# Kernel tuning notes

Measured on AMD Instinct MI355X. Metric: run time of the kernel, lower is better.

## Reference

```python
import jax, jax.numpy as jnp
import numpy as np

N_NODES = 50000
N_EDGES = 600000
IN_F = 128
HID_F = 128
OUT_F = 128


def setup_inputs() -> dict:
    key = jax.random.key(0)
    ks = jax.random.split(key, 12)
    features = jax.random.normal(ks[0], (N_NODES, IN_F), dtype=jnp.float32)
    src = jax.random.randint(ks[1], (N_EDGES,), 0, N_NODES, dtype=jnp.int32)
    dst = jax.random.randint(ks[2], (N_EDGES,), 0, N_NODES, dtype=jnp.int32)

    def lin(k, fan_in, fan_out):
        s = 1.0 / jnp.sqrt(fan_in)
        return jax.random.uniform(k, (fan_in, fan_out), jnp.float32, -s, s)

    return {
        "features": features, "src": src, "dst": dst,
        "W1_self": lin(ks[3], IN_F, HID_F), "W1_neigh": lin(ks[4], IN_F, HID_F),
        "b1": jnp.zeros((HID_F,), jnp.float32),
        "W2_self": lin(ks[5], HID_F, HID_F), "W2_neigh": lin(ks[6], HID_F, HID_F),
        "b2": jnp.zeros((HID_F,), jnp.float32),
        "W3_self": lin(ks[7], HID_F, OUT_F), "W3_neigh": lin(ks[8], HID_F, OUT_F),
        "b3": jnp.zeros((OUT_F,), jnp.float32),
    }


def _sage_mean(x, src, dst, W_self, W_neigh, b):
    # gather source-node features along edges, mean-reduce into dst nodes
    msgs = x[src]                                                # [E, d]
    summed = jax.ops.segment_sum(msgs, dst, num_segments=N_NODES)  # [N, d]
    deg = jax.ops.segment_sum(jnp.ones((dst.shape[0],), x.dtype), dst,
                              num_segments=N_NODES)               # [N]
    mean = summed / jnp.maximum(deg, 1.0)[:, None]
    return x @ W_self + mean @ W_neigh + b


def reference(features, src, dst,
              W1_self, W1_neigh, b1,
              W2_self, W2_neigh, b2,
              W3_self, W3_neigh, b3):
    x = features.reshape(features.shape[0], -1)  # Flatten (no-op for 2D)
    x = jax.nn.relu(_sage_mean(x, src, dst, W1_self, W1_neigh, b1))
    x = jax.nn.relu(_sage_mean(x, src, dst, W2_self, W2_neigh, b2))
    x = _sage_mean(x, src, dst, W3_self, W3_neigh, b3)
    return x
```

## Files before the change

kernel.cpp:

```cpp
#include <hip/hip_runtime.h>

#define NN 50000
#define NE 600000
#define F 128

typedef __attribute__((ext_vector_type(4))) float f4;
typedef __attribute__((ext_vector_type(4))) float f32x4;
typedef __bf16 bf16x8 __attribute__((ext_vector_type(8)));
typedef short short8v __attribute__((ext_vector_type(8)));
typedef unsigned short u16x4 __attribute__((ext_vector_type(4)));

__device__ inline ushort f2bf(float f) {
    uint u = __builtin_bit_cast(uint, f);
    uint r = (u + 0x7FFFu + ((u >> 16) & 1u)) >> 16;
    return (ushort)r;
}
__device__ inline float bf2f(ushort u) {
    uint t = ((uint)u) << 16;
    return __builtin_bit_cast(float, t);
}


__global__ void count_deg(const int* __restrict__ dst, int* __restrict__ deg, int E) {
    int e = blockIdx.x * blockDim.x + threadIdx.x;
    if (e < E) atomicAdd(&deg[dst[e]], 1);
}

__global__ __launch_bounds__(1024) void scan_part1(const int* __restrict__ deg,
                                                   int* __restrict__ bsum, int N) {
    __shared__ int ws[16];
    int tid = threadIdx.x;
    int idx = blockIdx.x * 1024 + tid;
    int v = (idx < N) ? deg[idx] : 0;
    #pragma unroll
    for (int o = 32; o; o >>= 1) v += __shfl_down(v, o);
    if ((tid & 63) == 0) ws[tid >> 6] = v;
    __syncthreads();
    if (tid < 64) {
        int t = (tid < 16) ? ws[tid] : 0;
        #pragma unroll
        for (int o = 8; o; o >>= 1) t += __shfl_down(t, o);
        if (tid == 0) bsum[blockIdx.x] = t;
    }
}

__global__ void scan_part2(int* __restrict__ bsum, int nb) {
    int lane = threadIdx.x;
    int v = (lane < nb) ? bsum[lane] : 0;
    int x = v;
    #pragma unroll
    for (int o = 1; o < 64; o <<= 1) {
        int t = __shfl_up(x, o);
        if (lane >= o) x += t;
    }
    if (lane < nb) bsum[lane] = x - v;
}

__global__ __launch_bounds__(1024) void scan_part3(const int* __restrict__ deg,
                                                   const int* __restrict__ bsum,
                                                   int* __restrict__ off,
                                                   int* __restrict__ cur,
                                                   float* __restrict__ recip, int N) {
    __shared__ int wsum[16];
    int tid = threadIdx.x;
    int wid = tid >> 6;
    int lane = tid & 63;
    int idx = blockIdx.x * 1024 + tid;
    int v = (idx < N) ? deg[idx] : 0;
    int x = v;
    #pragma unroll
    for (int o = 1; o < 64; o <<= 1) {
        int t = __shfl_up(x, o);
        if (lane >= o) x += t;
    }
    if (lane == 63) wsum[wid] = x;
    __syncthreads();
    if (tid == 0) {
        int a = 0;
        #pragma unroll
        for (int w = 0; w < 16; ++w) { int t = wsum[w]; wsum[w] = a; a += t; }
    }
    __syncthreads();
    int incl = x + wsum[wid];
    if (idx < N) {
        int start = bsum[blockIdx.x] + incl - v;
        off[idx] = start;
        cur[idx] = start;
        recip[idx] = 1.0f / (float)max(v, 1);
    }
}

__global__ void fill_csr(const int* __restrict__ src, const int* __restrict__ dst,
                         int* __restrict__ cur, int* __restrict__ csr, int E) {
    int e = blockIdx.x * blockDim.x + threadIdx.x;
    if (e < E) {
        int pos = atomicAdd(&cur[dst[e]], 1);
        csr[pos] = src[e];
    }
}


__global__ __launch_bounds__(256) void wt_prep(const float* __restrict__ W1s, const float* __restrict__ W1n,
                                               const float* __restrict__ W2s, const float* __restrict__ W2n,
                                               const float* __restrict__ W3s, const float* __restrict__ W3n,
                                               ushort* __restrict__ Bt1, ushort* __restrict__ Bt2,
                                               ushort* __restrict__ Bt3) {
    int layer = blockIdx.y;
    const float* Ws = (layer == 0) ? W1s : (layer == 1) ? W2s : W3s;
    const float* Wn = (layer == 0) ? W1n : (layer == 1) ? W2n : W3n;
    ushort* Bt = (layer == 0) ? Bt1 : (layer == 1) ? Bt2 : Bt3;
    int col = blockIdx.x;
    int k = threadIdx.x;
    float v = (k < 128) ? Ws[k * 128 + col] : Wn[(k - 128) * 128 + col];
    Bt[col * 256 + k] = f2bf(v);
}


__global__ __launch_bounds__(256) void to_bf16(const float* __restrict__ in,
                                               ushort* __restrict__ out, int n8) {
    int i = blockIdx.x * 256 + threadIdx.x;
    if (i < n8) {
        const f4* p = (const f4*)in + (size_t)i * 2;
        f4 a = p[0], b = p[1];
        short8v w;
        w[0] = (short)f2bf(a[0]); w[1] = (short)f2bf(a[1]);
        w[2] = (short)f2bf(a[2]); w[3] = (short)f2bf(a[3]);
        w[4] = (short)f2bf(b[0]); w[5] = (short)f2bf(b[1]);
        w[6] = (short)f2bf(b[2]); w[7] = (short)f2bf(b[3]);
        ((short8v*)out)[i] = w;
    }
}


__global__ __launch_bounds__(256) void agg_mean(const ushort* __restrict__ xb,
                                                const int* __restrict__ off,
                                                const int* __restrict__ deg,
                                                const float* __restrict__ recip,
                                                const int* __restrict__ csr,
                                                ushort* __restrict__ meanb, int N) {
    int node = blockIdx.x * 8 + (threadIdx.x >> 5);
    if (node >= N) return;
    int lane = threadIdx.x & 31;
    int start = off[node];
    int d = deg[node];
    const u16x4* xp = (const u16x4*)xb;
    f4 a = (f4)0.f;
    int nfull = d & ~7;
    int i = 0;
    for (; i < nfull; i += 8) {
        int s[8];
        #pragma unroll
        for (int u = 0; u < 8; ++u) s[u] = csr[start + i + u];
        u16x4 v[8];
        #pragma unroll
        for (int u = 0; u < 8; ++u) v[u] = xp[(size_t)s[u] * 32 + lane];
        #pragma unroll
        for (int u = 0; u < 8; ++u) {
            a[0] += bf2f(v[u][0]); a[1] += bf2f(v[u][1]);
            a[2] += bf2f(v[u][2]); a[3] += bf2f(v[u][3]);
        }
    }
    if (i < d) {
        int dm1 = d - 1;
        int s[8];
        #pragma unroll
        for (int u = 0; u < 8; ++u) {
            int idx = i + u;
            s[u] = csr[start + ((idx < dm1) ? idx : dm1)];
        }
        u16x4 v[8];
        #pragma unroll
        for (int u = 0; u < 8; ++u) v[u] = xp[(size_t)s[u] * 32 + lane];
        #pragma unroll
        for (int u = 0; u < 8; ++u) {
            float m = (i + u < d) ? 1.f : 0.f;
            a[0] += m * bf2f(v[u][0]); a[1] += m * bf2f(v[u][1]);
            a[2] += m * bf2f(v[u][2]); a[3] += m * bf2f(v[u][3]);
        }
    }
    float r = recip[node];
    u16x4 o;
    o[0] = f2bf(a[0] * r); o[1] = f2bf(a[1] * r);
    o[2] = f2bf(a[2] * r); o[3] = f2bf(a[3] * r);
    ((u16x4*)meanb)[(size_t)node * 32 + lane] = o;
}


template <int RELU, int OUTBF>
__global__ __launch_bounds__(256) void sage_gemm(const ushort* __restrict__ xb,
                                                 const ushort* __restrict__ meanb,
                                                 const ushort* __restrict__ Bt,
                                                 const float* __restrict__ bias,
                                                 void* __restrict__ outp, int N) {
    __shared__ ushort sa[32 * 256];
    int tid = threadIdx.x;
    int r0 = blockIdx.x * 32;

    {
        int row = tid >> 3;
        int kc = tid & 7;
        int grow = r0 + row;
        const ushort* srcp = (kc < 4) ? &xb[(size_t)grow * 128 + kc * 32]
                                      : &meanb[(size_t)grow * 128 + (kc - 4) * 32];
        uint base = (uint)(row * 512 + kc * 64);
        uint sw = ((uint)row & 7u) << 4;
        #pragma unroll
        for (int c = 0; c < 4; ++c) {
            short8v w;
            if (grow < N) w = ((const short8v*)srcp)[c];
            else          w = (short8v)0;
            *(short8v*)((char*)sa + ((base + c * 16) ^ sw)) = w;
        }
    }
    __syncthreads();

    int lane = tid & 63;
    int wid = tid >> 6;
    int wr = wid & 1;
    int wc = wid >> 1;
    int l15 = lane & 15;
    int lg = lane >> 4;

    int arow = wr * 16 + l15;
    uint abase = (uint)(arow * 512 + lg * 16);
    uint asw = ((uint)arow & 7u) << 4;
    bf16x8 a[8];
    #pragma unroll
    for (int ks = 0; ks < 8; ++ks) {
        a[ks] = *(const bf16x8*)((const char*)sa + ((abase + (uint)ks * 64) ^ asw));
    }

    f32x4 acc[4];
    #pragma unroll
    for (int ct = 0; ct < 4; ++ct) acc[ct] = (f32x4)0.f;

    #pragma unroll
    for (int ct = 0; ct < 4; ++ct) {
        int bcol = wc * 64 + ct * 16 + l15;
        const ushort* bp = Bt + bcol * 256 + lg * 8;
        #pragma unroll
        for (int ks = 0; ks < 8; ++ks) {
            bf16x8 b = *(const bf16x8*)(bp + ks * 32);
            acc[ct] = __builtin_amdgcn_mfma_f32_16x16x32_bf16(a[ks], b, acc[ct], 0, 0, 0);
        }
    }

    int crow = r0 + wr * 16 + lg * 4;
    #pragma unroll
    for (int ct = 0; ct < 4; ++ct) {
        int col = wc * 64 + ct * 16 + l15;
        float bv = bias[col];
        #pragma unroll
        for (int r = 0; r < 4; ++r) {
            int row = crow + r;
            if (row < N) {
                float v = acc[ct][r] + bv;
                if (RELU) v = fmaxf(v, 0.f);
                if (OUTBF) ((ushort*)outp)[(size_t)row * 128 + col] = f2bf(v);
                else       ((float*)outp)[(size_t)row * 128 + col] = v;
            }
        }
    }
}


extern "C" void kernel_launch(void* const* d_in, const int* in_sizes, int n_in,
                              void* d_out, int out_size, void* d_ws, size_t ws_size,
                              hipStream_t stream) {
    const float* feat = (const float*)d_in[0];
    const int* src = (const int*)d_in[1];
    const int* dst = (const int*)d_in[2];
    const float* W1s = (const float*)d_in[3];
    const float* W1n = (const float*)d_in[4];
    const float* b1 = (const float*)d_in[5];
    const float* W2s = (const float*)d_in[6];
    const float* W2n = (const float*)d_in[7];
    const float* b2 = (const float*)d_in[8];
    const float* W3s = (const float*)d_in[9];
    const float* W3n = (const float*)d_in[10];
    const float* b3 = (const float*)d_in[11];
    float* out = (float*)d_out;

    const int N = NN, E = NE;
    const int NB = (N + 1023) / 1024;

    char* p = (char*)d_ws;
    auto alloc = [&](size_t bytes) {
        char* q = p;
        p += (bytes + 255) & ~(size_t)255;
        return q;
    };
    int* deg = (int*)alloc((size_t)N * 4);
    int* off = (int*)alloc((size_t)N * 4);
    int* cur = (int*)alloc((size_t)N * 4);
    float* recip = (float*)alloc((size_t)N * 4);
    int* bsum = (int*)alloc(64 * 4);
    int* csr = (int*)alloc((size_t)E * 4);
    ushort* xb0 = (ushort*)alloc((size_t)N * F * 2);
    ushort* h1b = (ushort*)alloc((size_t)N * F * 2);
    ushort* h2b = (ushort*)alloc((size_t)N * F * 2);
    ushort* meanb = (ushort*)alloc((size_t)N * F * 2);
    ushort* Bt1 = (ushort*)alloc(128 * 256 * 2);
    ushort* Bt2 = (ushort*)alloc(128 * 256 * 2);
    ushort* Bt3 = (ushort*)alloc(128 * 256 * 2);

    wt_prep<<<dim3(128, 3), 256, 0, stream>>>(W1s, W1n, W2s, W2n, W3s, W3n, Bt1, Bt2, Bt3);
    to_bf16<<<(N * F / 8 + 255) / 256, 256, 0, stream>>>(feat, xb0, N * F / 8);

    hipMemsetAsync(deg, 0, (size_t)N * 4, stream);
    count_deg<<<(E + 255) / 256, 256, 0, stream>>>(dst, deg, E);
    scan_part1<<<NB, 1024, 0, stream>>>(deg, bsum, N);
    scan_part2<<<1, 64, 0, stream>>>(bsum, NB);
    scan_part3<<<NB, 1024, 0, stream>>>(deg, bsum, off, cur, recip, N);
    fill_csr<<<(E + 255) / 256, 256, 0, stream>>>(src, dst, cur, csr, E);

    int aggGrid = (N + 7) / 8;
    int gemmGrid = (N + 31) / 32;

    agg_mean<<<aggGrid, 256, 0, stream>>>(xb0, off, deg, recip, csr, meanb, N);
    sage_gemm<1, 1><<<gemmGrid, 256, 0, stream>>>(xb0, meanb, Bt1, b1, h1b, N);
    agg_mean<<<aggGrid, 256, 0, stream>>>(h1b, off, deg, recip, csr, meanb, N);
    sage_gemm<1, 1><<<gemmGrid, 256, 0, stream>>>(h1b, meanb, Bt2, b2, h2b, N);
    agg_mean<<<aggGrid, 256, 0, stream>>>(h2b, off, deg, recip, csr, meanb, N);
    sage_gemm<0, 0><<<gemmGrid, 256, 0, stream>>>(h2b, meanb, Bt3, b3, out, N);
}
```

Baseline: 253.4 us.

## Fuse mean aggregation into SAGE GEMM kernel and fold scan_part2 into scan_part3

Merges the separate mean-aggregation kernel into the GEMM kernel. Each block now gathers neighbour features for its 32 rows straight into shared memory, with 16 lanes per node using 16-byte loads, so the intermediate mean buffer is never written to or read back from global memory. The small scan_part2 launch is removed: each scan_part3 block recomputes the block-prefix over bsum itself. The cost is less parallelism during the gather (16 threads per node inside a GEMM-sized block), and the MFMA work now waits on the irregular gather latency.

```diff
diff --git a/kernel.cpp b/kernel.cpp
--- a/kernel.cpp
+++ b/kernel.cpp
@@ -8,7 +8,7 @@
 typedef __attribute__((ext_vector_type(4))) float f32x4;
 typedef __bf16 bf16x8 __attribute__((ext_vector_type(8)));
 typedef short short8v __attribute__((ext_vector_type(8)));
-typedef unsigned short u16x4 __attribute__((ext_vector_type(4)));
+typedef unsigned short u16x8 __attribute__((ext_vector_type(8)));
 
 __device__ inline ushort f2bf(float f) {
     uint u = __builtin_bit_cast(uint, f);
@@ -44,27 +44,27 @@
     }
 }
 
-__global__ void scan_part2(int* __restrict__ bsum, int nb) {
-    int lane = threadIdx.x;
-    int v = (lane < nb) ? bsum[lane] : 0;
-    int x = v;
-    #pragma unroll
-    for (int o = 1; o < 64; o <<= 1) {
-        int t = __shfl_up(x, o);
-        if (lane >= o) x += t;
-    }
-    if (lane < nb) bsum[lane] = x - v;
-}
-
 __global__ __launch_bounds__(1024) void scan_part3(const int* __restrict__ deg,
                                                    const int* __restrict__ bsum,
                                                    int* __restrict__ off,
                                                    int* __restrict__ cur,
-                                                   float* __restrict__ recip, int N) {
+                                                   float* __restrict__ recip,
+                                                   int N, int NB) {
     __shared__ int wsum[16];
+    __shared__ int sbase;
     int tid = threadIdx.x;
     int wid = tid >> 6;
     int lane = tid & 63;
+    if (tid < 64) {
+        int v = (tid < NB) ? bsum[tid] : 0;
+        int x = v;
+        #pragma unroll
+        for (int o = 1; o < 64; o <<= 1) {
+            int t = __shfl_up(x, o);
+            if (lane >= o) x += t;
+        }
+        if (tid == blockIdx.x) sbase = x - v;
+    }
     int idx = blockIdx.x * 1024 + tid;
     int v = (idx < N) ? deg[idx] : 0;
     int x = v;
@@ -83,7 +83,7 @@
     __syncthreads();
     int incl = x + wsum[wid];
     if (idx < N) {
-        int start = bsum[blockIdx.x] + incl - v;
+        int start = sbase + incl - v;
         off[idx] = start;
         cur[idx] = start;
         recip[idx] = 1.0f / (float)max(v, 1);
@@ -132,84 +132,89 @@
 }
 
 
-__global__ __launch_bounds__(256) void agg_mean(const ushort* __restrict__ xb,
-                                                const int* __restrict__ off,
-                                                const int* __restrict__ deg,
-                                                const float* __restrict__ recip,
-                                                const int* __restrict__ csr,
-                                                ushort* __restrict__ meanb, int N) {
-    int node = blockIdx.x * 8 + (threadIdx.x >> 5);
-    if (node >= N) return;
-    int lane = threadIdx.x & 31;
-    int start = off[node];
-    int d = deg[node];
-    const u16x4* xp = (const u16x4*)xb;
-    f4 a = (f4)0.f;
-    int nfull = d & ~7;
-    int i = 0;
-    for (; i < nfull; i += 8) {
-        int s[8];
-        #pragma unroll
-        for (int u = 0; u < 8; ++u) s[u] = csr[start + i + u];
-        u16x4 v[8];
-        #pragma unroll
-        for (int u = 0; u < 8; ++u) v[u] = xp[(size_t)s[u] * 32 + lane];
-        #pragma unroll
-        for (int u = 0; u < 8; ++u) {
-            a[0] += bf2f(v[u][0]); a[1] += bf2f(v[u][1]);
-            a[2] += bf2f(v[u][2]); a[3] += bf2f(v[u][3]);
-        }
-    }
-    if (i < d) {
-        int dm1 = d - 1;
-        int s[8];
-        #pragma unroll
-        for (int u = 0; u < 8; ++u) {
-            int idx = i + u;
-            s[u] = csr[start + ((idx < dm1) ? idx : dm1)];
-        }
-        u16x4 v[8];
-        #pragma unroll
-        for (int u = 0; u < 8; ++u) v[u] = xp[(size_t)s[u] * 32 + lane];
-        #pragma unroll
-        for (int u = 0; u < 8; ++u) {
-            float m = (i + u < d) ? 1.f : 0.f;
-            a[0] += m * bf2f(v[u][0]); a[1] += m * bf2f(v[u][1]);
-            a[2] += m * bf2f(v[u][2]); a[3] += m * bf2f(v[u][3]);
-        }
-    }
-    float r = recip[node];
-    u16x4 o;
-    o[0] = f2bf(a[0] * r); o[1] = f2bf(a[1] * r);
-    o[2] = f2bf(a[2] * r); o[3] = f2bf(a[3] * r);
-    ((u16x4*)meanb)[(size_t)node * 32 + lane] = o;
-}
-
-
 template <int RELU, int OUTBF>
-__global__ __launch_bounds__(256) void sage_gemm(const ushort* __restrict__ xb,
-                                                 const ushort* __restrict__ meanb,
-                                                 const ushort* __restrict__ Bt,
-                                                 const float* __restrict__ bias,
-                                                 void* __restrict__ outp, int N) {
+__global__ __launch_bounds__(256) void sage_layer(const ushort* __restrict__ xb,
+                                                  const int* __restrict__ off,
+                                                  const int* __restrict__ deg,
+                                                  const float* __restrict__ recip,
+                                                  const int* __restrict__ csr,
+                                                  const ushort* __restrict__ Bt,
+                                                  const float* __restrict__ bias,
+                                                  void* __restrict__ outp, int N) {
     __shared__ ushort sa[32 * 256];
     int tid = threadIdx.x;
     int r0 = blockIdx.x * 32;
 
     {
         int row = tid >> 3;
-        int kc = tid & 7;
+        int c = tid & 7;
         int grow = r0 + row;
-        const ushort* srcp = (kc < 4) ? &xb[(size_t)grow * 128 + kc * 32]
-                                      : &meanb[(size_t)grow * 128 + (kc - 4) * 32];
-        uint base = (uint)(row * 512 + kc * 64);
         uint sw = ((uint)row & 7u) << 4;
-        #pragma unroll
-        for (int c = 0; c < 4; ++c) {
+        uint base = (uint)(row * 512 + c * 32);
+        short8v w0 = (short8v)0, w1 = (short8v)0;
+        if (grow < N) {
+            const short8v* sp = (const short8v*)&xb[(size_t)grow * 128 + c * 16];
+            w0 = sp[0]; w1 = sp[1];
+        }
+        *(short8v*)((char*)sa + (base ^ sw)) = w0;
+        *(short8v*)((char*)sa + ((base + 16) ^ sw)) = w1;
+    }
+
+    {
+        int g = tid >> 4;
+        int l16 = tid & 15;
+        const ushort* xpb = xb + (size_t)l16 * 8;
+        #pragma unroll
+        for (int rep = 0; rep < 2; ++rep) {
+            int row = g + rep * 16;
+            int node = r0 + row;
+            float a[8] = {0.f, 0.f, 0.f, 0.f, 0.f, 0.f, 0.f, 0.f};
+            if (node < N) {
+                int start = off[node];
+                int d = deg[node];
+                int nfull = d & ~7;
+                int i = 0;
+                for (; i < nfull; i += 8) {
+                    int s[8];
+                    #pragma unroll
+                    for (int u = 0; u < 8; ++u) s[u] = csr[start + i + u];
+                    u16x8 v[8];
+                    #pragma unroll
+                    for (int u = 0; u < 8; ++u) v[u] = *(const u16x8*)(xpb + (size_t)s[u] * 128);
+                    #pragma unroll
+                    for (int u = 0; u < 8; ++u) {
+                        #pragma unroll
+                        for (int j = 0; j < 8; ++j) a[j] += bf2f(v[u][j]);
+                    }
+                }
+                if (i < d) {
+                    int dm1 = d - 1;
+                    int s[8];
+                    #pragma unroll
+                    for (int u = 0; u < 8; ++u) {
+                        int idx = i + u;
+                        s[u] = csr[start + ((idx < dm1) ? idx : dm1)];
+                    }
+                    u16x8 v[8];
+                    #pragma unroll
+                    for (int u = 0; u < 8; ++u) v[u] = *(const u16x8*)(xpb + (size_t)s[u] * 128);
+                    #pragma unroll
+                    for (int u = 0; u < 8; ++u) {
+                        float m = (i + u < d) ? 1.f : 0.f;
+                        #pragma unroll
+                        for (int j = 0; j < 8; ++j) a[j] += m * bf2f(v[u][j]);
+                    }
+                }
+                float r = recip[node];
+                #pragma unroll
+                for (int j = 0; j < 8; ++j) a[j] *= r;
+            }
             short8v w;
-            if (grow < N) w = ((const short8v*)srcp)[c];
-            else          w = (short8v)0;
-            *(short8v*)((char*)sa + ((base + c * 16) ^ sw)) = w;
+            #pragma unroll
+            for (int j = 0; j < 8; ++j) w[j] = (short)f2bf(a[j]);
+            uint sw = ((uint)row & 7u) << 4;
+            uint addr = (uint)(row * 512 + 256 + l16 * 16);
+            *(short8v*)((char*)sa + (addr ^ sw)) = w;
         }
     }
     __syncthreads();
@@ -299,7 +304,6 @@
     ushort* xb0 = (ushort*)alloc((size_t)N * F * 2);
     ushort* h1b = (ushort*)alloc((size_t)N * F * 2);
     ushort* h2b = (ushort*)alloc((size_t)N * F * 2);
-    ushort* meanb = (ushort*)alloc((size_t)N * F * 2);
     ushort* Bt1 = (ushort*)alloc(128 * 256 * 2);
     ushort* Bt2 = (ushort*)alloc(128 * 256 * 2);
     ushort* Bt3 = (ushort*)alloc(128 * 256 * 2);
@@ -310,17 +314,12 @@
     hipMemsetAsync(deg, 0, (size_t)N * 4, stream);
     count_deg<<<(E + 255) / 256, 256, 0, stream>>>(dst, deg, E);
     scan_part1<<<NB, 1024, 0, stream>>>(deg, bsum, N);
-    scan_part2<<<1, 64, 0, stream>>>(bsum, NB);
-    scan_part3<<<NB, 1024, 0, stream>>>(deg, bsum, off, cur, recip, N);
+    scan_part3<<<NB, 1024, 0, stream>>>(deg, bsum, off, cur, recip, N, NB);
     fill_csr<<<(E + 255) / 256, 256, 0, stream>>>(src, dst, cur, csr, E);
 
-    int aggGrid = (N + 7) / 8;
-    int gemmGrid = (N + 31) / 32;
-
-    agg_mean<<<aggGrid, 256, 0, stream>>>(xb0, off, deg, recip, csr, meanb, N);
-    sage_gemm<1, 1><<<gemmGrid, 256, 0, stream>>>(xb0, meanb, Bt1, b1, h1b, N);
-    agg_mean<<<aggGrid, 256, 0, stream>>>(h1b, off, deg, recip, csr, meanb, N);
-    sage_gemm<1, 1><<<gemmGrid, 256, 0, stream>>>(h1b, meanb, Bt2, b2, h2b, N);
-    agg_mean<<<aggGrid, 256, 0, stream>>>(h2b, off, deg, recip, csr, meanb, N);
-    sage_gemm<0, 0><<<gemmGrid, 256, 0, stream>>>(h2b, meanb, Bt3, b3, out, N);
-}
+    int grid = (N + 31) / 32;
+
+    sage_layer<1, 1><<<grid, 256, 0, stream>>>(xb0, off, deg, recip, csr, Bt1, b1, h1b, N);
+    sage_layer<1, 1><<<grid, 256, 0, stream>>>(h1b, off, deg, recip, csr, Bt2, b2, h2b, N);
+    sage_layer<0, 0><<<grid, 256, 0, stream>>>(h2b, off, deg, recip, csr, Bt3, b3, out, N);
+}
```

Result: faster. 244.3 us, median of 2 (-3.6%).

## Aggregate per-thread node over feature chunks and fold block-sum scan into scan_part3

Applied to the files above, without the earlier changes.

The mean aggregation changes from 32 lanes per node (each reading 8 bytes) to one thread per node handling a 16-feature chunk, with the grid split across 8 feature chunks. Each thread now loads two 16-byte vectors per neighbor and keeps 16 accumulators. Coalescing across a warp's gathers is lost, but this may improve cache-line reuse across chunk blocks and raise per-thread memory-level parallelism. Separately, the single-block scan over block sums is removed; each scan_part3 block recomputes the prefix of bsum itself, saving one kernel launch.

```diff
diff --git a/kernel.cpp b/kernel.cpp
--- a/kernel.cpp
+++ b/kernel.cpp
@@ -8,7 +8,7 @@
 typedef __attribute__((ext_vector_type(4))) float f32x4;
 typedef __bf16 bf16x8 __attribute__((ext_vector_type(8)));
 typedef short short8v __attribute__((ext_vector_type(8)));
-typedef unsigned short u16x4 __attribute__((ext_vector_type(4)));
+typedef unsigned short u16x8 __attribute__((ext_vector_type(8)));
 
 __device__ inline ushort f2bf(float f) {
     uint u = __builtin_bit_cast(uint, f);
@@ -44,27 +44,27 @@
     }
 }
 
-__global__ void scan_part2(int* __restrict__ bsum, int nb) {
-    int lane = threadIdx.x;
-    int v = (lane < nb) ? bsum[lane] : 0;
-    int x = v;
-    #pragma unroll
-    for (int o = 1; o < 64; o <<= 1) {
-        int t = __shfl_up(x, o);
-        if (lane >= o) x += t;
-    }
-    if (lane < nb) bsum[lane] = x - v;
-}
-
 __global__ __launch_bounds__(1024) void scan_part3(const int* __restrict__ deg,
                                                    const int* __restrict__ bsum,
                                                    int* __restrict__ off,
                                                    int* __restrict__ cur,
-                                                   float* __restrict__ recip, int N) {
+                                                   float* __restrict__ recip,
+                                                   int N, int NB) {
     __shared__ int wsum[16];
+    __shared__ int sbase;
     int tid = threadIdx.x;
     int wid = tid >> 6;
     int lane = tid & 63;
+    if (tid < 64) {
+        int v = (tid < NB) ? bsum[tid] : 0;
+        int x = v;
+        #pragma unroll
+        for (int o = 1; o < 64; o <<= 1) {
+            int t = __shfl_up(x, o);
+            if (lane >= o) x += t;
+        }
+        if (tid == blockIdx.x) sbase = x - v;
+    }
     int idx = blockIdx.x * 1024 + tid;
     int v = (idx < N) ? deg[idx] : 0;
     int x = v;
@@ -83,7 +83,7 @@
     __syncthreads();
     int incl = x + wsum[wid];
     if (idx < N) {
-        int start = bsum[blockIdx.x] + incl - v;
+        int start = sbase + incl - v;
         off[idx] = start;
         cur[idx] = start;
         recip[idx] = 1.0f / (float)max(v, 1);
@@ -132,32 +132,41 @@
 }
 
 
-__global__ __launch_bounds__(256) void agg_mean(const ushort* __restrict__ xb,
-                                                const int* __restrict__ off,
-                                                const int* __restrict__ deg,
-                                                const float* __restrict__ recip,
-                                                const int* __restrict__ csr,
-                                                ushort* __restrict__ meanb, int N) {
-    int node = blockIdx.x * 8 + (threadIdx.x >> 5);
+__global__ __launch_bounds__(256) void agg_chunk(const ushort* __restrict__ xb,
+                                                 const int* __restrict__ off,
+                                                 const int* __restrict__ deg,
+                                                 const float* __restrict__ recip,
+                                                 const int* __restrict__ csr,
+                                                 ushort* __restrict__ meanb, int N) {
+    int chunk = blockIdx.x;
+    int node = blockIdx.y * 256 + threadIdx.x;
     if (node >= N) return;
-    int lane = threadIdx.x & 31;
+    const ushort* xc = xb + chunk * 16;
     int start = off[node];
     int d = deg[node];
-    const u16x4* xp = (const u16x4*)xb;
-    f4 a = (f4)0.f;
+    float a[16];
+    #pragma unroll
+    for (int j = 0; j < 16; ++j) a[j] = 0.f;
     int nfull = d & ~7;
     int i = 0;
     for (; i < nfull; i += 8) {
         int s[8];
         #pragma unroll
         for (int u = 0; u < 8; ++u) s[u] = csr[start + i + u];
-        u16x4 v[8];
-        #pragma unroll
-        for (int u = 0; u < 8; ++u) v[u] = xp[(size_t)s[u] * 32 + lane];
-        #pragma unroll
-        for (int u = 0; u < 8; ++u) {
-            a[0] += bf2f(v[u][0]); a[1] += bf2f(v[u][1]);
-            a[2] += bf2f(v[u][2]); a[3] += bf2f(v[u][3]);
+        u16x8 v0[8], v1[8];
+        #pragma unroll
+        for (int u = 0; u < 8; ++u) {
+            const ushort* r = xc + (size_t)s[u] * 128;
+            v0[u] = *(const u16x8*)r;
+            v1[u] = *(const u16x8*)(r + 8);
+        }
+        #pragma unroll
+        for (int u = 0; u < 8; ++u) {
+            #pragma unroll
+            for (int j = 0; j < 8; ++j) {
+                a[j] += bf2f(v0[u][j]);
+                a[8 + j] += bf2f(v1[u][j]);
+            }
         }
     }
     if (i < d) {
@@ -168,21 +177,33 @@
             int idx = i + u;
             s[u] = csr[start + ((idx < dm1) ? idx : dm1)];
         }
-        u16x4 v[8];
-        #pragma unroll
-        for (int u = 0; u < 8; ++u) v[u] = xp[(size_t)s[u] * 32 + lane];
+        u16x8 v0[8], v1[8];
+        #pragma unroll
+        for (int u = 0; u < 8; ++u) {
+            const ushort* r = xc + (size_t)s[u] * 128;
+            v0[u] = *(const u16x8*)r;
+            v1[u] = *(const u16x8*)(r + 8);
+        }
         #pragma unroll
         for (int u = 0; u < 8; ++u) {
             float m = (i + u < d) ? 1.f : 0.f;
-            a[0] += m * bf2f(v[u][0]); a[1] += m * bf2f(v[u][1]);
-            a[2] += m * bf2f(v[u][2]); a[3] += m * bf2f(v[u][3]);
+            #pragma unroll
+            for (int j = 0; j < 8; ++j) {
+                a[j] += m * bf2f(v0[u][j]);
+                a[8 + j] += m * bf2f(v1[u][j]);
+            }
         }
     }
     float r = recip[node];
-    u16x4 o;
-    o[0] = f2bf(a[0] * r); o[1] = f2bf(a[1] * r);
-    o[2] = f2bf(a[2] * r); o[3] = f2bf(a[3] * r);
-    ((u16x4*)meanb)[(size_t)node * 32 + lane] = o;
+    u16x8 o0, o1;
+    #pragma unroll
+    for (int j = 0; j < 8; ++j) {
+        o0[j] = f2bf(a[j] * r);
+        o1[j] = f2bf(a[8 + j] * r);
+    }
+    ushort* mp = meanb + (size_t)node * 128 + chunk * 16;
+    *(u16x8*)mp = o0;
+    *(u16x8*)(mp + 8) = o1;
 }
 
 
@@ -310,17 +331,16 @@
     hipMemsetAsync(deg, 0, (size_t)N * 4, stream);
     count_deg<<<(E + 255) / 256, 256, 0, stream>>>(dst, deg, E);
     scan_part1<<<NB, 1024, 0, stream>>>(deg, bsum, N);
-    scan_part2<<<1, 64, 0, stream>>>(bsum, NB);
-    scan_part3<<<NB, 1024, 0, stream>>>(deg, bsum, off, cur, recip, N);
+    scan_part3<<<NB, 1024, 0, stream>>>(deg, bsum, off, cur, recip, N, NB);
     fill_csr<<<(E + 255) / 256, 256, 0, stream>>>(src, dst, cur, csr, E);
 
-    int aggGrid = (N + 7) / 8;
+    dim3 aggGrid(8, (N + 255) / 256);
     int gemmGrid = (N + 31) / 32;
 
-    agg_mean<<<aggGrid, 256, 0, stream>>>(xb0, off, deg, recip, csr, meanb, N);
+    agg_chunk<<<aggGrid, 256, 0, stream>>>(xb0, off, deg, recip, csr, meanb, N);
     sage_gemm<1, 1><<<gemmGrid, 256, 0, stream>>>(xb0, meanb, Bt1, b1, h1b, N);
-    agg_mean<<<aggGrid, 256, 0, stream>>>(h1b, off, deg, recip, csr, meanb, N);
+    agg_chunk<<<aggGrid, 256, 0, stream>>>(h1b, off, deg, recip, csr, meanb, N);
     sage_gemm<1, 1><<<gemmGrid, 256, 0, stream>>>(h1b, meanb, Bt2, b2, h2b, N);
-    agg_mean<<<aggGrid, 256, 0, stream>>>(h2b, off, deg, recip, csr, meanb, N);
+    agg_chunk<<<aggGrid, 256, 0, stream>>>(h2b, off, deg, recip, csr, meanb, N);
     sage_gemm<0, 0><<<gemmGrid, 256, 0, stream>>>(h2b, meanb, Bt3, b3, out, N);
 }
```

Result: slower. 376.7 us (+48.6%).
